# Optimization experiments

Hardware: AMD Instinct MI355X
Metric: run time of the kernel (lower is better)

Reference implementation:

```python
import jax, jax.numpy as jnp
from jax import lax
import numpy as np

D_MODEL, D_STATE, EXPAND, D_CONV = 1024, 16, 2, 4
D_INNER = EXPAND * D_MODEL
B, L = 4, 2048


def setup_inputs() -> dict:
    key = jax.random.key(0)
    ks = jax.random.split(key, 12)
    def xavier(k, shape):
        fan_in, fan_out = shape[1], shape[0]
        lim = float(np.sqrt(6.0 / (fan_in + fan_out)))
        return jax.random.uniform(k, shape, jnp.float32, -lim, lim)
    inp = {}
    inp['x'] = jax.random.normal(ks[0], (B, L, D_MODEL), jnp.float32)
    inp['W_left'] = xavier(ks[1], (D_INNER, D_MODEL))
    inp['conv_w'] = jax.random.normal(ks[2], (D_INNER, 1, D_CONV), jnp.float32) * (1.0 / np.sqrt(D_CONV))
    inp['conv_b'] = jax.random.normal(ks[3], (D_INNER,), jnp.float32) * 0.01
    inp['W_delta'] = jax.random.normal(ks[4], (D_INNER, D_INNER), jnp.float32) * (1.0 / np.sqrt(D_INNER))
    inp['b_delta'] = jnp.zeros((D_INNER,), jnp.float32)
    inp['W_B'] = jax.random.normal(ks[5], (D_STATE, D_INNER), jnp.float32) * (1.0 / np.sqrt(D_INNER))
    inp['W_C'] = jax.random.normal(ks[6], (D_STATE, D_INNER), jnp.float32) * (1.0 / np.sqrt(D_INNER))
    inp['A_log'] = jnp.log(jnp.arange(1, D_STATE + 1, dtype=jnp.float32))
    inp['W_right'] = xavier(ks[7], (D_INNER, D_MODEL))
    inp['ln_g'] = jnp.ones((D_INNER,), jnp.float32)
    inp['ln_b'] = jnp.zeros((D_INNER,), jnp.float32)
    inp['W_out'] = xavier(ks[8], (D_MODEL, D_INNER))
    return inp


def _ssm(xl, W_delta, b_delta, W_B, W_C, A_log):
    # xl: [b, l, d_inner]
    b, l, d_inner = xl.shape
    A = -jax.nn.softplus(A_log)  # [d_state]
    delta = jnp.clip(jax.nn.softplus(xl @ W_delta.T + b_delta), 1e-4, 10.0)
    Bm = xl @ W_B.T  # [b, l, d_state]
    Cm = xl @ W_C.T  # [b, l, d_state]

    def step(h, inp):
        d_t, x_t, B_t, C_t = inp  # [b,d_inner], [b,d_inner], [b,N], [b,N]
        A_bar = jnp.exp(d_t[:, :, None] * A)            # [b, d_inner, N]
        h = A_bar * h + (d_t * x_t)[:, :, None] * B_t[:, None, :]
        y_t = jnp.einsum('bdn,bn->bd', h, C_t)
        return h, y_t

    h0 = jnp.zeros((b, d_inner, A_log.shape[0]), xl.dtype)
    xs = (jnp.swapaxes(delta, 0, 1), jnp.swapaxes(xl, 0, 1),
          jnp.swapaxes(Bm, 0, 1), jnp.swapaxes(Cm, 0, 1))
    _, ys = lax.scan(step, h0, xs)  # ys: [l, b, d_inner]
    return jnp.swapaxes(ys, 0, 1)


def reference(x, W_left, conv_w, conv_b, W_delta, b_delta, W_B, W_C, A_log,
              W_right, ln_g, ln_b, W_out):
    d_conv = conv_w.shape[-1]
    # left branch: linear -> causal depthwise conv1d -> silu
    left = x @ W_left.T                          # [b, l, d_inner]
    left_ncw = jnp.swapaxes(left, 1, 2)          # [b, d_inner, l]
    left_ncw = jnp.pad(left_ncw, ((0, 0), (0, 0), (d_conv - 1, 0)))
    left_ncw = lax.conv_general_dilated(
        left_ncw, conv_w, window_strides=(1,), padding='VALID',
        feature_group_count=conv_w.shape[0]) + conv_b[None, :, None]
    left = jax.nn.silu(jnp.swapaxes(left_ncw, 1, 2))
    # selective scan
    ssm_out = _ssm(left, W_delta, b_delta, W_B, W_C, A_log)
    # right gate (eval mode: dropout off)
    gate = jax.nn.silu(x @ W_right.T)
    out = ssm_out * gate
    # layernorm over d_inner
    mu = jnp.mean(out, axis=-1, keepdims=True)
    var = jnp.mean(jnp.square(out - mu), axis=-1, keepdims=True)
    out = (out - mu) * lax.rsqrt(var + 1e-5) * ln_g + ln_b
    return out @ W_out.T
```

## Files before the change

kernel.cpp:

```cpp
#include <hip/hip_runtime.h>
#include <cstddef>

#define LL 2048
#define TOK 8192
#define DM 1024
#define DI 2048
#define NS 16

typedef _Float16 half_t;
typedef __attribute__((ext_vector_type(8))) _Float16 f16x8;
typedef __attribute__((ext_vector_type(4))) _Float16 f16x4;
typedef __attribute__((ext_vector_type(4))) float f32x4;

__device__ __forceinline__ float softplus_f(float x) {
  return fmaxf(x, 0.f) + log1pf(__expf(-fabsf(x)));
}
__device__ __forceinline__ float silu_f(float x) {
  return x / (1.f + __expf(-x));
}
__device__ __forceinline__ void gload_lds16(const void* g, void* l) {
  __builtin_amdgcn_global_load_lds((const __attribute__((address_space(1))) void*)g,
                                   (__attribute__((address_space(3))) void*)l, 16, 0, 0);
}
#define DPP_ADD(v, ctrl) \
  ((v) + __int_as_float(__builtin_amdgcn_update_dpp(0, __float_as_int(v), (ctrl), 0xf, 0xf, true)))

__device__ float g_buf[120881152];

__global__ __launch_bounds__(256) void f2h_k(const float* __restrict__ in,
                                             half_t* __restrict__ out, int n4) {
  const int i = blockIdx.x * 256 + threadIdx.x;
  if (i >= n4) return;
  const float4 v = ((const float4*)in)[i];
  f16x4 o;
  o[0] = (half_t)v.x; o[1] = (half_t)v.y; o[2] = (half_t)v.z; o[3] = (half_t)v.w;
  ((f16x4*)out)[i] = o;
}

__global__ __launch_bounds__(256) void f2h2_k(const float* __restrict__ in,
                                              half_t* __restrict__ hi,
                                              half_t* __restrict__ lo, int n4) {
  const int i = blockIdx.x * 256 + threadIdx.x;
  if (i >= n4) return;
  const float4 v = ((const float4*)in)[i];
  f16x4 h, l;
  h[0] = (half_t)v.x; h[1] = (half_t)v.y; h[2] = (half_t)v.z; h[3] = (half_t)v.w;
  l[0] = (half_t)(v.x - (float)h[0]);
  l[1] = (half_t)(v.y - (float)h[1]);
  l[2] = (half_t)(v.z - (float)h[2]);
  l[3] = (half_t)(v.w - (float)h[3]);
  ((f16x4*)hi)[i] = h;
  ((f16x4*)lo)[i] = l;
}

template <int ACT>
__global__ __launch_bounds__(256) void gemm_mfma(const half_t* __restrict__ A,
                                                 const half_t* __restrict__ W,
                                                 const float* __restrict__ bias,
                                                 float* __restrict__ C,
                                                 int M, int N, int K) {
  __shared__ half_t lA[4096];
  __shared__ half_t lB[4096];
  const int tid = threadIdx.x;
  const int bm0 = blockIdx.y * 128, bn0 = blockIdx.x * 128;
  const int lane = tid & 63, wave = tid >> 6;
  const int q = lane >> 4, mr = lane & 15;
  const int wm = (wave >> 1) * 64, wn = (wave & 1) * 64;
  const int flat0 = tid, flat1 = tid + 256;
  const int kc0 = flat0 >> 7, r0 = flat0 & 127;
  const int kc1 = flat1 >> 7, r1 = flat1 & 127;

  f32x4 acc[4][4];
#pragma unroll
  for (int i = 0; i < 4; ++i)
#pragma unroll
    for (int j = 0; j < 4; ++j) acc[i][j] = (f32x4){0.f, 0.f, 0.f, 0.f};

  for (int k0 = 0; k0 < K; k0 += 32) {
    gload_lds16(A + (size_t)(bm0 + r0) * K + k0 + kc0 * 8, lA + (size_t)flat0 * 8);
    gload_lds16(A + (size_t)(bm0 + r1) * K + k0 + kc1 * 8, lA + (size_t)flat1 * 8);
    gload_lds16(W + (size_t)(bn0 + r0) * K + k0 + kc0 * 8, lB + (size_t)flat0 * 8);
    gload_lds16(W + (size_t)(bn0 + r1) * K + k0 + kc1 * 8, lB + (size_t)flat1 * 8);
    __syncthreads();
    f16x8 af[4], bg[4];
#pragma unroll
    for (int t = 0; t < 4; ++t) {
      af[t] = *(const f16x8*)(lA + ((q << 10) + ((wm + t * 16 + mr) << 3)));
      bg[t] = *(const f16x8*)(lB + ((q << 10) + ((wn + t * 16 + mr) << 3)));
    }
#pragma unroll
    for (int i = 0; i < 4; ++i)
#pragma unroll
      for (int j = 0; j < 4; ++j)
        acc[i][j] = __builtin_amdgcn_mfma_f32_16x16x32_f16(af[i], bg[j], acc[i][j], 0, 0, 0);
    __syncthreads();
  }

#pragma unroll
  for (int i = 0; i < 4; ++i) {
#pragma unroll
    for (int j = 0; j < 4; ++j) {
      const int col = bn0 + wn + j * 16 + mr;
      const float bv = bias ? bias[col] : 0.f;
#pragma unroll
      for (int r = 0; r < 4; ++r) {
        const int row = bm0 + wm + i * 16 + q * 4 + r;
        float v = acc[i][j][r] + bv;
        if (ACT == 1) v = silu_f(v);
        C[(size_t)row * N + col] = v;
      }
    }
  }
}

__global__ __launch_bounds__(256) void gemm_mfma_lg(const half_t* __restrict__ A,
                                                    const half_t* __restrict__ W,
                                                    float* __restrict__ left,
                                                    float* __restrict__ gate) {
  __shared__ half_t lA[4096];
  __shared__ half_t lB[4096];
  const int tid = threadIdx.x;
  const int bm0 = blockIdx.y * 128, bn0 = blockIdx.x * 128;
  const int K = DM;
  const int lane = tid & 63, wave = tid >> 6;
  const int q = lane >> 4, mr = lane & 15;
  const int wm = (wave >> 1) * 64, wn = (wave & 1) * 64;
  const int flat1 = tid + 256;
  const int kc0 = tid >> 7, r0 = tid & 127;
  const int kc1 = flat1 >> 7, r1 = flat1 & 127;

  f32x4 acc[4][4];
#pragma unroll
  for (int i = 0; i < 4; ++i)
#pragma unroll
    for (int j = 0; j < 4; ++j) acc[i][j] = (f32x4){0.f, 0.f, 0.f, 0.f};

  for (int k0 = 0; k0 < K; k0 += 32) {
    gload_lds16(A + (size_t)(bm0 + r0) * K + k0 + kc0 * 8, lA + (size_t)tid * 8);
    gload_lds16(A + (size_t)(bm0 + r1) * K + k0 + kc1 * 8, lA + (size_t)flat1 * 8);
    gload_lds16(W + (size_t)(bn0 + r0) * K + k0 + kc0 * 8, lB + (size_t)tid * 8);
    gload_lds16(W + (size_t)(bn0 + r1) * K + k0 + kc1 * 8, lB + (size_t)flat1 * 8);
    __syncthreads();
    f16x8 af[4], bg[4];
#pragma unroll
    for (int t = 0; t < 4; ++t) {
      af[t] = *(const f16x8*)(lA + ((q << 10) + ((wm + t * 16 + mr) << 3)));
      bg[t] = *(const f16x8*)(lB + ((q << 10) + ((wn + t * 16 + mr) << 3)));
    }
#pragma unroll
    for (int i = 0; i < 4; ++i)
#pragma unroll
      for (int j = 0; j < 4; ++j)
        acc[i][j] = __builtin_amdgcn_mfma_f32_16x16x32_f16(af[i], bg[j], acc[i][j], 0, 0, 0);
    __syncthreads();
  }

  const int is_gate = (bn0 >= DI);
  float* out = is_gate ? gate : left;
  const int cb = bn0 - (is_gate ? DI : 0);
#pragma unroll
  for (int i = 0; i < 4; ++i) {
#pragma unroll
    for (int j = 0; j < 4; ++j) {
      const int col = cb + wn + j * 16 + mr;
#pragma unroll
      for (int r = 0; r < 4; ++r) {
        const int row = bm0 + wm + i * 16 + q * 4 + r;
        float v = acc[i][j][r];
        if (is_gate) v = silu_f(v);
        out[(size_t)row * DI + col] = v;
      }
    }
  }
}

__global__ __launch_bounds__(512, 4) void gemm_mfma_split(const half_t* __restrict__ Ah,
                                                          const half_t* __restrict__ Wh,
                                                          const half_t* __restrict__ Wl,
                                                          const float* __restrict__ bias,
                                                          float* __restrict__ C,
                                                          int M, int N, int K) {
  __shared__ half_t lAh[8192];
  __shared__ half_t lBh[4096], lBl[4096];
  const int tid = threadIdx.x;
  const int bm0 = blockIdx.y * 256, bn0 = blockIdx.x * 128;
  const int lane = tid & 63, wave = tid >> 6;
  const int q = lane >> 4, mr = lane & 15;
  const int wm = (wave >> 1) * 64, wn = (wave & 1) * 64;
  const int aflat1 = tid + 512;
  const int akc0 = tid >> 8, ar0 = tid & 255;
  const int akc1 = aflat1 >> 8, ar1 = aflat1 & 255;
  const int wkc = tid >> 7, wr = tid & 127;

  f32x4 acc[4][4];
#pragma unroll
  for (int i = 0; i < 4; ++i)
#pragma unroll
    for (int j = 0; j < 4; ++j) acc[i][j] = (f32x4){0.f, 0.f, 0.f, 0.f};

  for (int k0 = 0; k0 < K; k0 += 32) {
    gload_lds16(Ah + (size_t)(bm0 + ar0) * K + k0 + akc0 * 8, lAh + (size_t)tid * 8);
    gload_lds16(Ah + (size_t)(bm0 + ar1) * K + k0 + akc1 * 8, lAh + (size_t)aflat1 * 8);
    gload_lds16(Wh + (size_t)(bn0 + wr) * K + k0 + wkc * 8, lBh + (size_t)tid * 8);
    gload_lds16(Wl + (size_t)(bn0 + wr) * K + k0 + wkc * 8, lBl + (size_t)tid * 8);
    __syncthreads();
    f16x8 ah[4], bh[4], bl[4];
#pragma unroll
    for (int t = 0; t < 4; ++t) {
      const int ao = (q << 11) + ((wm + t * 16 + mr) << 3);
      const int bo = (q << 10) + ((wn + t * 16 + mr) << 3);
      ah[t] = *(const f16x8*)(lAh + ao);
      bh[t] = *(const f16x8*)(lBh + bo);
      bl[t] = *(const f16x8*)(lBl + bo);
    }
#pragma unroll
    for (int i = 0; i < 4; ++i)
#pragma unroll
      for (int j = 0; j < 4; ++j) {
        acc[i][j] = __builtin_amdgcn_mfma_f32_16x16x32_f16(ah[i], bh[j], acc[i][j], 0, 0, 0);
        acc[i][j] = __builtin_amdgcn_mfma_f32_16x16x32_f16(ah[i], bl[j], acc[i][j], 0, 0, 0);
      }
    __syncthreads();
  }

  const int wmg = (wave >> 1) * 64;
#pragma unroll
  for (int i = 0; i < 4; ++i) {
#pragma unroll
    for (int j = 0; j < 4; ++j) {
      const int col = bn0 + wn + j * 16 + mr;
      const float bv = bias[col];
#pragma unroll
      for (int r = 0; r < 4; ++r) {
        const int row = bm0 + wmg + i * 16 + q * 4 + r;
        float v = softplus_f(acc[i][j][r] + bv);
        v = fminf(fmaxf(v, 1e-4f), 10.f);
        C[(size_t)row * N + col] = v;
      }
    }
  }
}

__global__ __launch_bounds__(256) void bc_mfma(const half_t* __restrict__ A,
                                               const half_t* __restrict__ Wbc,
                                               float* __restrict__ bc) {
  __shared__ half_t lA[4096];
  __shared__ half_t lB[1024];
  const int tid = threadIdx.x;
  const int bm0 = blockIdx.x * 128;
  const int lane = tid & 63, wave = tid >> 6;
  const int q = lane >> 4, mr = lane & 15;
  const int wm = wave * 32;
  const int flat1 = tid + 256;
  const int kcA0 = tid >> 7, rA0 = tid & 127;
  const int kcA1 = flat1 >> 7, rA1 = flat1 & 127;
  const int kcB = tid >> 5, rB = tid & 31;

  f32x4 acc[2][2];
#pragma unroll
  for (int i = 0; i < 2; ++i)
#pragma unroll
    for (int j = 0; j < 2; ++j) acc[i][j] = (f32x4){0.f, 0.f, 0.f, 0.f};

  for (int k0 = 0; k0 < DI; k0 += 32) {
    gload_lds16(A + (size_t)(bm0 + rA0) * DI + k0 + kcA0 * 8, lA + (size_t)tid * 8);
    gload_lds16(A + (size_t)(bm0 + rA1) * DI + k0 + kcA1 * 8, lA + (size_t)flat1 * 8);
    if (tid < 128)
      gload_lds16(Wbc + (size_t)rB * DI + k0 + kcB * 8, lB + (size_t)tid * 8);
    __syncthreads();
    f16x8 af[2], bg[2];
#pragma unroll
    for (int t = 0; t < 2; ++t) {
      af[t] = *(const f16x8*)(lA + ((q << 10) + ((wm + t * 16 + mr) << 3)));
      bg[t] = *(const f16x8*)(lB + ((q << 8) + ((t * 16 + mr) << 3)));
    }
#pragma unroll
    for (int i = 0; i < 2; ++i)
#pragma unroll
      for (int j = 0; j < 2; ++j)
        acc[i][j] = __builtin_amdgcn_mfma_f32_16x16x32_f16(af[i], bg[j], acc[i][j], 0, 0, 0);
    __syncthreads();
  }

#pragma unroll
  for (int i = 0; i < 2; ++i) {
#pragma unroll
    for (int j = 0; j < 2; ++j) {
#pragma unroll
      for (int r = 0; r < 4; ++r) {
        const int row = bm0 + wm + i * 16 + q * 4 + r;
        bc[(size_t)row * 32 + 2 * mr + j] = acc[i][j][r];
      }
    }
  }
}

__global__ __launch_bounds__(256) void conv_silu_k(const float* __restrict__ left,
                                                   const float* __restrict__ cw,
                                                   const float* __restrict__ cb,
                                                   float* __restrict__ xc,
                                                   half_t* __restrict__ xch) {
  const int idx = blockIdx.x * 256 + threadIdx.x;
  const int d = idx & (DI - 1);
  const int bt = idx >> 11;
  const int t = bt & (LL - 1);
  const float4 wv = *(const float4*)(cw + (size_t)d * 4);
  float acc = cb[d];
  const size_t base = (size_t)idx;
  if (t >= 3) {
    acc += left[base - 3 * DI] * wv.x + left[base - 2 * DI] * wv.y +
           left[base - DI] * wv.z + left[base] * wv.w;
  } else {
    acc += left[base] * wv.w;
    if (t >= 1) acc += left[base - DI] * wv.z;
    if (t >= 2) acc += left[base - 2 * DI] * wv.y;
  }
  const float v = silu_f(acc);
  xc[base] = v;
  xch[base] = (half_t)v;
}

#define ST 32
__global__ __launch_bounds__(256) void scan_k(const float* __restrict__ delta,
                                              const float* __restrict__ xc,
                                              const float* __restrict__ gate,
                                              const float* __restrict__ bcp,
                                              const float* __restrict__ A_log,
                                              float* __restrict__ y) {
  __shared__ float dx2[16 * 68];
  __shared__ float bcs[ST * 32];
  __shared__ float ys[ST * 16];
  const int tid = threadIdx.x;
  const int b  = blockIdx.x >> 7;
  const int d0 = (blockIdx.x & 127) << 4;
  const int n  = tid & 15;
  const int ch = tid >> 4;
  const float An = -softplus_f(A_log[n]);

  const int t_a = tid >> 4, c_a = tid & 15;
  const int t_b = t_a + 16;

  float h = 0.f;
  const size_t batch_base = (size_t)b * LL * DI + d0;
  const size_t batch_bc   = (size_t)b * LL * 32;

  size_t rb_cur = batch_base;
  float g0, g1;
  {
    const size_t ra = rb_cur + (size_t)t_a * DI + c_a;
    const size_t rbx = rb_cur + (size_t)t_b * DI + c_a;
    const float d0v = delta[ra], x0v = xc[ra];
    const float d1v = delta[rbx], x1v = xc[rbx];
    g0 = gate[ra]; g1 = gate[rbx];
    const float2 b0 = *(const float2*)&bcp[batch_bc + (size_t)t_a * 32 + 2 * c_a];
    const float2 b1 = *(const float2*)&bcp[batch_bc + (size_t)t_b * 32 + 2 * c_a];
    *(float2*)&dx2[c_a * 68 + t_a * 2] = make_float2(d0v, x0v);
    *(float2*)&dx2[c_a * 68 + t_b * 2] = make_float2(d1v, x1v);
    *(float2*)&bcs[t_a * 32 + 2 * c_a] = b0;
    *(float2*)&bcs[t_b * 32 + 2 * c_a] = b1;
  }
  __syncthreads();

  for (int it = 0; it < LL / ST; ++it) {
    float nd0, nx0, ng0, nd1, nx1, ng1;
    float2 nb0, nb1;
    const size_t rb_nxt = batch_base + (size_t)(it + 1) * ST * DI;
    if (it + 1 < LL / ST) {
      const size_t ra = rb_nxt + (size_t)t_a * DI + c_a;
      const size_t rbx = rb_nxt + (size_t)t_b * DI + c_a;
      nd0 = delta[ra]; nx0 = xc[ra]; ng0 = gate[ra];
      nd1 = delta[rbx]; nx1 = xc[rbx]; ng1 = gate[rbx];
      const size_t bcb = batch_bc + (size_t)(it + 1) * ST * 32;
      nb0 = *(const float2*)&bcp[bcb + (size_t)t_a * 32 + 2 * c_a];
      nb1 = *(const float2*)&bcp[bcb + (size_t)t_b * 32 + 2 * c_a];
    }

    const float* dxp = &dx2[ch * 68];
#pragma unroll
    for (int tt = 0; tt < ST; tt += 2) {
      const float4 v = *(const float4*)&dxp[tt * 2];
      const float2 bc0 = *(const float2*)&bcs[tt * 32 + 2 * n];
      const float2 bc1 = *(const float2*)&bcs[(tt + 1) * 32 + 2 * n];
      float ab = __expf(v.x * An);
      h = fmaf(ab, h, v.x * v.y * bc0.x);
      float p = h * bc0.y;
      p = DPP_ADD(p, 0x111); p = DPP_ADD(p, 0x112);
      p = DPP_ADD(p, 0x114); p = DPP_ADD(p, 0x118);
      if (n == 15) ys[tt * 16 + ch] = p;
      ab = __expf(v.z * An);
      h = fmaf(ab, h, v.z * v.w * bc1.x);
      p = h * bc1.y;
      p = DPP_ADD(p, 0x111); p = DPP_ADD(p, 0x112);
      p = DPP_ADD(p, 0x114); p = DPP_ADD(p, 0x118);
      if (n == 15) ys[(tt + 1) * 16 + ch] = p;
    }
    __syncthreads();

    if (it + 1 < LL / ST) {
      *(float2*)&dx2[c_a * 68 + t_a * 2] = make_float2(nd0, nx0);
      *(float2*)&dx2[c_a * 68 + t_b * 2] = make_float2(nd1, nx1);
      *(float2*)&bcs[t_a * 32 + 2 * c_a] = nb0;
      *(float2*)&bcs[t_b * 32 + 2 * c_a] = nb1;
    }
    y[rb_cur + (size_t)t_a * DI + c_a] = ys[t_a * 16 + c_a] * g0;
    y[rb_cur + (size_t)t_b * DI + c_a] = ys[t_b * 16 + c_a] * g1;
    g0 = ng0; g1 = ng1;
    rb_cur = rb_nxt;
    __syncthreads();
  }
}

__global__ __launch_bounds__(256) void ln_k(const float* __restrict__ y,
                                            const float* __restrict__ gam,
                                            const float* __restrict__ bet,
                                            half_t* __restrict__ outn) {
  const int row = blockIdx.x;
  const int tid = threadIdx.x;
  const float* yr = y + (size_t)row * DI;
  const float4 v0 = ((const float4*)yr)[tid];
  const float4 v1 = ((const float4*)yr)[tid + 256];
  float s = v0.x + v0.y + v0.z + v0.w + v1.x + v1.y + v1.z + v1.w;
  float q = v0.x * v0.x + v0.y * v0.y + v0.z * v0.z + v0.w * v0.w +
            v1.x * v1.x + v1.y * v1.y + v1.z * v1.z + v1.w * v1.w;
  for (int off = 32; off > 0; off >>= 1) {
    s += __shfl_down(s, off);
    q += __shfl_down(q, off);
  }
  __shared__ float sred[4], qred[4];
  const int wid = tid >> 6;
  if ((tid & 63) == 0) { sred[wid] = s; qred[wid] = q; }
  __syncthreads();
  s = sred[0] + sred[1] + sred[2] + sred[3];
  q = qred[0] + qred[1] + qred[2] + qred[3];
  const float mu = s * (1.f / DI);
  const float rs = rsqrtf(q * (1.f / DI) - mu * mu + 1e-5f);
  half_t* orow = outn + (size_t)row * DI;
  const int c0 = tid * 4, c1 = (tid + 256) * 4;
  f16x4 o;
  o[0] = (half_t)((v0.x - mu) * rs * gam[c0 + 0] + bet[c0 + 0]);
  o[1] = (half_t)((v0.y - mu) * rs * gam[c0 + 1] + bet[c0 + 1]);
  o[2] = (half_t)((v0.z - mu) * rs * gam[c0 + 2] + bet[c0 + 2]);
  o[3] = (half_t)((v0.w - mu) * rs * gam[c0 + 3] + bet[c0 + 3]);
  ((f16x4*)orow)[tid] = o;
  o[0] = (half_t)((v1.x - mu) * rs * gam[c1 + 0] + bet[c1 + 0]);
  o[1] = (half_t)((v1.y - mu) * rs * gam[c1 + 1] + bet[c1 + 1]);
  o[2] = (half_t)((v1.z - mu) * rs * gam[c1 + 2] + bet[c1 + 2]);
  o[3] = (half_t)((v1.w - mu) * rs * gam[c1 + 3] + bet[c1 + 3]);
  ((f16x4*)orow)[tid + 256] = o;
}

extern "C" void kernel_launch(void* const* d_in, const int* in_sizes, int n_in,
                              void* d_out, int out_size, void* d_ws, size_t ws_size,
                              hipStream_t stream) {
  const float* x       = (const float*)d_in[0];
  const float* W_left  = (const float*)d_in[1];
  const float* conv_w  = (const float*)d_in[2];
  const float* conv_b  = (const float*)d_in[3];
  const float* W_delta = (const float*)d_in[4];
  const float* b_delta = (const float*)d_in[5];
  const float* W_B     = (const float*)d_in[6];
  const float* W_C     = (const float*)d_in[7];
  const float* A_log   = (const float*)d_in[8];
  const float* W_right = (const float*)d_in[9];
  const float* ln_g    = (const float*)d_in[10];
  const float* ln_b    = (const float*)d_in[11];
  const float* W_out   = (const float*)d_in[12];

  float* buf = nullptr;
  hipGetSymbolAddress((void**)&buf, HIP_SYMBOL(g_buf));
  half_t* xh   = (half_t*)(buf + 0);
  half_t* wlgh = (half_t*)(buf + 4194304);
  half_t* wrh  = (half_t*)(buf + 5242880);
  half_t* wdh  = (half_t*)(buf + 6291456);
  half_t* wdl  = (half_t*)(buf + 8388608);
  half_t* woh  = (half_t*)(buf + 10485760);
  float* left  = buf + 11534336;
  float* xc    = buf + 28311552;
  half_t* xch  = (half_t*)(buf + 45088768);
  float* dlt   = buf + 61865984;
  float* gate  = buf + 78643200;
  float* yv    = buf + 95420416;
  half_t* nrmh = (half_t*)(buf + 112197632);
  float* bc    = buf + 120586240;
  half_t* wbch = (half_t*)(buf + 120848384);

  f2h_k<<<8192, 256, 0, stream>>>(x, xh, TOK * DM / 4);
  f2h_k<<<2048, 256, 0, stream>>>(W_left, wlgh, DI * DM / 4);
  f2h_k<<<2048, 256, 0, stream>>>(W_right, wrh, DI * DM / 4);
  f2h_k<<<2048, 256, 0, stream>>>(W_out, woh, DM * DI / 4);
  f2h2_k<<<4096, 256, 0, stream>>>(W_delta, wdh, wdl, DI * DI / 4);
  f2h_k<<<32, 256, 0, stream>>>(W_B, wbch, NS * DI / 4);
  f2h_k<<<32, 256, 0, stream>>>(W_C, wbch + NS * DI, NS * DI / 4);

  gemm_mfma_lg<<<dim3(2 * DI / 128, TOK / 128), 256, 0, stream>>>(xh, wlgh, left, gate);
  conv_silu_k<<<TOK * DI / 256, 256, 0, stream>>>(left, conv_w, conv_b, xc, xch);
  gemm_mfma_split<<<dim3(DI / 128, TOK / 256), 512, 0, stream>>>(xch, wdh, wdl, b_delta, dlt, TOK, DI, DI);
  bc_mfma<<<TOK / 128, 256, 0, stream>>>(xch, wbch, bc);
  scan_k<<<512, 256, 0, stream>>>(dlt, xc, gate, bc, A_log, yv);
  ln_k<<<TOK, 256, 0, stream>>>(yv, ln_g, ln_b, nrmh);
  gemm_mfma<0><<<dim3(DM / 128, TOK / 128), 256, 0, stream>>>(nrmh, woh, nullptr, (float*)d_out, TOK, DM, DI);
}
```

Measured before the change: 930.4 us.

## Double-buffer and enlarge delta split-GEMM tile to 256x256 with MFMA priority

```diff
diff --git a/kernel.cpp b/kernel.cpp
--- a/kernel.cpp
+++ b/kernel.cpp
@@ -174,65 +174,87 @@
   }
 }
 
-__global__ __launch_bounds__(512, 4) void gemm_mfma_split(const half_t* __restrict__ Ah,
+__global__ __launch_bounds__(512, 2) void gemm_mfma_split(const half_t* __restrict__ Ah,
                                                           const half_t* __restrict__ Wh,
                                                           const half_t* __restrict__ Wl,
                                                           const float* __restrict__ bias,
                                                           float* __restrict__ C,
                                                           int M, int N, int K) {
-  __shared__ half_t lAh[8192];
-  __shared__ half_t lBh[4096], lBl[4096];
+  __shared__ half_t lAh[2][8192];
+  __shared__ half_t lBh[2][8192];
+  __shared__ half_t lBl[2][8192];
   const int tid = threadIdx.x;
-  const int bm0 = blockIdx.y * 256, bn0 = blockIdx.x * 128;
+  const int bm0 = blockIdx.y * 256, bn0 = blockIdx.x * 256;
   const int lane = tid & 63, wave = tid >> 6;
   const int q = lane >> 4, mr = lane & 15;
-  const int wm = (wave >> 1) * 64, wn = (wave & 1) * 64;
-  const int aflat1 = tid + 512;
-  const int akc0 = tid >> 8, ar0 = tid & 255;
-  const int akc1 = aflat1 >> 8, ar1 = aflat1 & 255;
-  const int wkc = tid >> 7, wr = tid & 127;
-
-  f32x4 acc[4][4];
-#pragma unroll
-  for (int i = 0; i < 4; ++i)
+  const int wm = (wave >> 2) * 128, wn = (wave & 3) * 64;
+  const int f0 = tid, f1 = tid + 512;
+  const int kc0 = f0 >> 8, r0 = f0 & 255;
+  const int kc1 = f1 >> 8, r1 = f1 & 255;
+
+#define STAGE_S(bufp, kk)                                                            \
+  do {                                                                               \
+    gload_lds16(Ah + (size_t)(bm0 + r0) * K + (kk) + kc0 * 8, lAh[bufp] + f0 * 8);   \
+    gload_lds16(Ah + (size_t)(bm0 + r1) * K + (kk) + kc1 * 8, lAh[bufp] + f1 * 8);   \
+    gload_lds16(Wh + (size_t)(bn0 + r0) * K + (kk) + kc0 * 8, lBh[bufp] + f0 * 8);   \
+    gload_lds16(Wh + (size_t)(bn0 + r1) * K + (kk) + kc1 * 8, lBh[bufp] + f1 * 8);   \
+    gload_lds16(Wl + (size_t)(bn0 + r0) * K + (kk) + kc0 * 8, lBl[bufp] + f0 * 8);   \
+    gload_lds16(Wl + (size_t)(bn0 + r1) * K + (kk) + kc1 * 8, lBl[bufp] + f1 * 8);   \
+  } while (0)
+
+  f32x4 acc[8][4];
+#pragma unroll
+  for (int i = 0; i < 8; ++i)
 #pragma unroll
     for (int j = 0; j < 4; ++j) acc[i][j] = (f32x4){0.f, 0.f, 0.f, 0.f};
 
+  STAGE_S(0, 0);
+  __syncthreads();
+
+  int cur = 0;
   for (int k0 = 0; k0 < K; k0 += 32) {
-    gload_lds16(Ah + (size_t)(bm0 + ar0) * K + k0 + akc0 * 8, lAh + (size_t)tid * 8);
-    gload_lds16(Ah + (size_t)(bm0 + ar1) * K + k0 + akc1 * 8, lAh + (size_t)aflat1 * 8);
-    gload_lds16(Wh + (size_t)(bn0 + wr) * K + k0 + wkc * 8, lBh + (size_t)tid * 8);
-    gload_lds16(Wl + (size_t)(bn0 + wr) * K + k0 + wkc * 8, lBl + (size_t)tid * 8);
-    __syncthreads();
-    f16x8 ah[4], bh[4], bl[4];
-#pragma unroll
-    for (int t = 0; t < 4; ++t) {
-      const int ao = (q << 11) + ((wm + t * 16 + mr) << 3);
-      const int bo = (q << 10) + ((wn + t * 16 + mr) << 3);
-      ah[t] = *(const f16x8*)(lAh + ao);
-      bh[t] = *(const f16x8*)(lBh + bo);
-      bl[t] = *(const f16x8*)(lBl + bo);
-    }
-#pragma unroll
-    for (int i = 0; i < 4; ++i)
-#pragma unroll
-      for (int j = 0; j < 4; ++j) {
-        acc[i][j] = __builtin_amdgcn_mfma_f32_16x16x32_f16(ah[i], bh[j], acc[i][j], 0, 0, 0);
-        acc[i][j] = __builtin_amdgcn_mfma_f32_16x16x32_f16(ah[i], bl[j], acc[i][j], 0, 0, 0);
-      }
-    __syncthreads();
-  }
-
-  const int wmg = (wave >> 1) * 64;
-#pragma unroll
-  for (int i = 0; i < 4; ++i) {
+    if (k0 + 32 < K) STAGE_S(cur ^ 1, k0 + 32);
+
+    const int qb = q << 11;
+    const f16x8* pA = (const f16x8*)(lAh[cur] + qb);
+    const f16x8* pBh = (const f16x8*)(lBh[cur] + qb);
+    const f16x8* pBl = (const f16x8*)(lBl[cur] + qb);
+    f16x8 ah[8], bh4[4], bl4[4];
+#pragma unroll
+    for (int j = 0; j < 4; ++j) {
+      bh4[j] = pBh[wn + j * 16 + mr];
+      bl4[j] = pBl[wn + j * 16 + mr];
+    }
+#pragma unroll
+    for (int i = 0; i < 8; ++i) ah[i] = pA[wm + i * 16 + mr];
+
+    __builtin_amdgcn_s_setprio(1);
+#pragma unroll
+    for (int i = 0; i < 8; ++i)
+#pragma unroll
+      for (int j = 0; j < 4; ++j)
+        acc[i][j] = __builtin_amdgcn_mfma_f32_16x16x32_f16(ah[i], bh4[j], acc[i][j], 0, 0, 0);
+#pragma unroll
+    for (int i = 0; i < 8; ++i)
+#pragma unroll
+      for (int j = 0; j < 4; ++j)
+        acc[i][j] = __builtin_amdgcn_mfma_f32_16x16x32_f16(ah[i], bl4[j], acc[i][j], 0, 0, 0);
+    __builtin_amdgcn_s_setprio(0);
+
+    __syncthreads();
+    cur ^= 1;
+  }
+#undef STAGE_S
+
+#pragma unroll
+  for (int i = 0; i < 8; ++i) {
 #pragma unroll
     for (int j = 0; j < 4; ++j) {
       const int col = bn0 + wn + j * 16 + mr;
       const float bv = bias[col];
 #pragma unroll
       for (int r = 0; r < 4; ++r) {
-        const int row = bm0 + wmg + i * 16 + q * 4 + r;
+        const int row = bm0 + wm + i * 16 + q * 4 + r;
         float v = softplus_f(acc[i][j][r] + bv);
         v = fminf(fmaxf(v, 1e-4f), 10.f);
         C[(size_t)row * N + col] = v;
@@ -494,7 +516,7 @@
 
   gemm_mfma_lg<<<dim3(2 * DI / 128, TOK / 128), 256, 0, stream>>>(xh, wlgh, left, gate);
   conv_silu_k<<<TOK * DI / 256, 256, 0, stream>>>(left, conv_w, conv_b, xc, xch);
-  gemm_mfma_split<<<dim3(DI / 128, TOK / 256), 512, 0, stream>>>(xch, wdh, wdl, b_delta, dlt, TOK, DI, DI);
+  gemm_mfma_split<<<dim3(DI / 256, TOK / 256), 512, 0, stream>>>(xch, wdh, wdl, b_delta, dlt, TOK, DI, DI);
   bc_mfma<<<TOK / 128, 256, 0, stream>>>(xch, wbch, bc);
   scan_k<<<512, 256, 0, stream>>>(dlt, xc, gate, bc, A_log, yv);
   ln_k<<<TOK, 256, 0, stream>>>(yv, ln_g, ln_b, nrmh);
```

Result: slower. 1.637 ms (+75.9%).

## Retile delta GEMM to 128x128 blocks with swizzled block order and MFMA priority

Applied to the files above, without the earlier changes.

```diff
diff --git a/kernel.cpp b/kernel.cpp
--- a/kernel.cpp
+++ b/kernel.cpp
@@ -174,23 +174,26 @@
   }
 }
 
-__global__ __launch_bounds__(512, 4) void gemm_mfma_split(const half_t* __restrict__ Ah,
+__global__ __launch_bounds__(256, 4) void gemm_mfma_split(const half_t* __restrict__ Ah,
                                                           const half_t* __restrict__ Wh,
                                                           const half_t* __restrict__ Wl,
                                                           const float* __restrict__ bias,
                                                           float* __restrict__ C,
                                                           int M, int N, int K) {
-  __shared__ half_t lAh[8192];
-  __shared__ half_t lBh[4096], lBl[4096];
+  __shared__ half_t lA[4096];
+  __shared__ half_t lBh[4096];
+  __shared__ half_t lBl[4096];
   const int tid = threadIdx.x;
-  const int bm0 = blockIdx.y * 256, bn0 = blockIdx.x * 128;
+  const int flat = blockIdx.y * gridDim.x + blockIdx.x;
+  const int lo = (flat >> 3) | ((flat & 7) << 7);
+  const int bn0 = (lo & 15) << 7;
+  const int bm0 = (lo >> 4) << 7;
   const int lane = tid & 63, wave = tid >> 6;
   const int q = lane >> 4, mr = lane & 15;
   const int wm = (wave >> 1) * 64, wn = (wave & 1) * 64;
-  const int aflat1 = tid + 512;
-  const int akc0 = tid >> 8, ar0 = tid & 255;
-  const int akc1 = aflat1 >> 8, ar1 = aflat1 & 255;
-  const int wkc = tid >> 7, wr = tid & 127;
+  const int flat1 = tid + 256;
+  const int kc0 = tid >> 7, r0 = tid & 127;
+  const int kc1 = flat1 >> 7, r1 = flat1 & 127;
 
   f32x4 acc[4][4];
 #pragma unroll
@@ -199,31 +202,34 @@
     for (int j = 0; j < 4; ++j) acc[i][j] = (f32x4){0.f, 0.f, 0.f, 0.f};
 
   for (int k0 = 0; k0 < K; k0 += 32) {
-    gload_lds16(Ah + (size_t)(bm0 + ar0) * K + k0 + akc0 * 8, lAh + (size_t)tid * 8);
-    gload_lds16(Ah + (size_t)(bm0 + ar1) * K + k0 + akc1 * 8, lAh + (size_t)aflat1 * 8);
-    gload_lds16(Wh + (size_t)(bn0 + wr) * K + k0 + wkc * 8, lBh + (size_t)tid * 8);
-    gload_lds16(Wl + (size_t)(bn0 + wr) * K + k0 + wkc * 8, lBl + (size_t)tid * 8);
-    __syncthreads();
-    f16x8 ah[4], bh[4], bl[4];
+    gload_lds16(Ah + (size_t)(bm0 + r0) * K + k0 + kc0 * 8, lA + (size_t)tid * 8);
+    gload_lds16(Ah + (size_t)(bm0 + r1) * K + k0 + kc1 * 8, lA + (size_t)flat1 * 8);
+    gload_lds16(Wh + (size_t)(bn0 + r0) * K + k0 + kc0 * 8, lBh + (size_t)tid * 8);
+    gload_lds16(Wh + (size_t)(bn0 + r1) * K + k0 + kc1 * 8, lBh + (size_t)flat1 * 8);
+    gload_lds16(Wl + (size_t)(bn0 + r0) * K + k0 + kc0 * 8, lBl + (size_t)tid * 8);
+    gload_lds16(Wl + (size_t)(bn0 + r1) * K + k0 + kc1 * 8, lBl + (size_t)flat1 * 8);
+    __syncthreads();
+    f16x8 af[4], bh[4], bl[4];
 #pragma unroll
     for (int t = 0; t < 4; ++t) {
-      const int ao = (q << 11) + ((wm + t * 16 + mr) << 3);
-      const int bo = (q << 10) + ((wn + t * 16 + mr) << 3);
-      ah[t] = *(const f16x8*)(lAh + ao);
-      bh[t] = *(const f16x8*)(lBh + bo);
-      bl[t] = *(const f16x8*)(lBl + bo);
-    }
+      const int o = (q << 10) + ((wm + t * 16 + mr) << 3);
+      const int ob = (q << 10) + ((wn + t * 16 + mr) << 3);
+      af[t] = *(const f16x8*)(lA + o);
+      bh[t] = *(const f16x8*)(lBh + ob);
+      bl[t] = *(const f16x8*)(lBl + ob);
+    }
+    __builtin_amdgcn_s_setprio(1);
 #pragma unroll
     for (int i = 0; i < 4; ++i)
 #pragma unroll
       for (int j = 0; j < 4; ++j) {
-        acc[i][j] = __builtin_amdgcn_mfma_f32_16x16x32_f16(ah[i], bh[j], acc[i][j], 0, 0, 0);
-        acc[i][j] = __builtin_amdgcn_mfma_f32_16x16x32_f16(ah[i], bl[j], acc[i][j], 0, 0, 0);
+        acc[i][j] = __builtin_amdgcn_mfma_f32_16x16x32_f16(af[i], bh[j], acc[i][j], 0, 0, 0);
+        acc[i][j] = __builtin_amdgcn_mfma_f32_16x16x32_f16(af[i], bl[j], acc[i][j], 0, 0, 0);
       }
-    __syncthreads();
-  }
-
-  const int wmg = (wave >> 1) * 64;
+    __builtin_amdgcn_s_setprio(0);
+    __syncthreads();
+  }
+
 #pragma unroll
   for (int i = 0; i < 4; ++i) {
 #pragma unroll
@@ -232,7 +238,7 @@
       const float bv = bias[col];
 #pragma unroll
       for (int r = 0; r < 4; ++r) {
-        const int row = bm0 + wmg + i * 16 + q * 4 + r;
+        const int row = bm0 + wm + i * 16 + q * 4 + r;
         float v = softplus_f(acc[i][j][r] + bv);
         v = fminf(fmaxf(v, 1e-4f), 10.f);
         C[(size_t)row * N + col] = v;
@@ -494,7 +500,7 @@
 
   gemm_mfma_lg<<<dim3(2 * DI / 128, TOK / 128), 256, 0, stream>>>(xh, wlgh, left, gate);
   conv_silu_k<<<TOK * DI / 256, 256, 0, stream>>>(left, conv_w, conv_b, xc, xch);
-  gemm_mfma_split<<<dim3(DI / 128, TOK / 256), 512, 0, stream>>>(xch, wdh, wdl, b_delta, dlt, TOK, DI, DI);
+  gemm_mfma_split<<<dim3(DI / 128, TOK / 128), 256, 0, stream>>>(xch, wdh, wdl, b_delta, dlt, TOK, DI, DI);
   bc_mfma<<<TOK / 128, 256, 0, stream>>>(xch, wbch, bc);
   scan_k<<<512, 256, 0, stream>>>(dlt, xc, gate, bc, A_log, yv);
   ln_k<<<TOK, 256, 0, stream>>>(yv, ln_g, ln_b, nrmh);
```

New measurement: 1.013 ms. +8.9%, slower.

## Drop hi/lo split for delta GEMM and fuse B/C projection into it

Applied to the files above, without the earlier changes.

```diff
diff --git a/kernel.cpp b/kernel.cpp
--- a/kernel.cpp
+++ b/kernel.cpp
@@ -37,20 +37,12 @@
   ((f16x4*)out)[i] = o;
 }
 
-__global__ __launch_bounds__(256) void f2h2_k(const float* __restrict__ in,
-                                              half_t* __restrict__ hi,
-                                              half_t* __restrict__ lo, int n4) {
+__global__ __launch_bounds__(256) void zh_k(half_t* __restrict__ out, int n4) {
   const int i = blockIdx.x * 256 + threadIdx.x;
   if (i >= n4) return;
-  const float4 v = ((const float4*)in)[i];
-  f16x4 h, l;
-  h[0] = (half_t)v.x; h[1] = (half_t)v.y; h[2] = (half_t)v.z; h[3] = (half_t)v.w;
-  l[0] = (half_t)(v.x - (float)h[0]);
-  l[1] = (half_t)(v.y - (float)h[1]);
-  l[2] = (half_t)(v.z - (float)h[2]);
-  l[3] = (half_t)(v.w - (float)h[3]);
-  ((f16x4*)hi)[i] = h;
-  ((f16x4*)lo)[i] = l;
+  f16x4 o;
+  o[0] = (half_t)0.f; o[1] = (half_t)0.f; o[2] = (half_t)0.f; o[3] = (half_t)0.f;
+  ((f16x4*)out)[i] = o;
 }
 
 template <int ACT>
@@ -174,16 +166,16 @@
   }
 }
 
-__global__ __launch_bounds__(512, 4) void gemm_mfma_split(const half_t* __restrict__ Ah,
-                                                          const half_t* __restrict__ Wh,
-                                                          const half_t* __restrict__ Wl,
-                                                          const float* __restrict__ bias,
-                                                          float* __restrict__ C,
-                                                          int M, int N, int K) {
-  __shared__ half_t lAh[8192];
-  __shared__ half_t lBh[4096], lBl[4096];
+__global__ __launch_bounds__(512, 4) void gemm_delta_bc(const half_t* __restrict__ A,
+                                                        const half_t* __restrict__ W,
+                                                        const float* __restrict__ bias,
+                                                        float* __restrict__ dlt,
+                                                        float* __restrict__ bcout) {
+  __shared__ half_t lA[8192];
+  __shared__ half_t lB[4096];
   const int tid = threadIdx.x;
   const int bm0 = blockIdx.y * 256, bn0 = blockIdx.x * 128;
+  const int K = DI;
   const int lane = tid & 63, wave = tid >> 6;
   const int q = lane >> 4, mr = lane & 15;
   const int wm = (wave >> 1) * 64, wn = (wave & 1) * 64;
@@ -199,97 +191,58 @@
     for (int j = 0; j < 4; ++j) acc[i][j] = (f32x4){0.f, 0.f, 0.f, 0.f};
 
   for (int k0 = 0; k0 < K; k0 += 32) {
-    gload_lds16(Ah + (size_t)(bm0 + ar0) * K + k0 + akc0 * 8, lAh + (size_t)tid * 8);
-    gload_lds16(Ah + (size_t)(bm0 + ar1) * K + k0 + akc1 * 8, lAh + (size_t)aflat1 * 8);
-    gload_lds16(Wh + (size_t)(bn0 + wr) * K + k0 + wkc * 8, lBh + (size_t)tid * 8);
-    gload_lds16(Wl + (size_t)(bn0 + wr) * K + k0 + wkc * 8, lBl + (size_t)tid * 8);
-    __syncthreads();
-    f16x8 ah[4], bh[4], bl[4];
+    gload_lds16(A + (size_t)(bm0 + ar0) * K + k0 + akc0 * 8, lA + (size_t)tid * 8);
+    gload_lds16(A + (size_t)(bm0 + ar1) * K + k0 + akc1 * 8, lA + (size_t)aflat1 * 8);
+    gload_lds16(W + (size_t)(bn0 + wr) * K + k0 + wkc * 8, lB + (size_t)tid * 8);
+    __syncthreads();
+    f16x8 ah[4], bg[4];
 #pragma unroll
     for (int t = 0; t < 4; ++t) {
       const int ao = (q << 11) + ((wm + t * 16 + mr) << 3);
       const int bo = (q << 10) + ((wn + t * 16 + mr) << 3);
-      ah[t] = *(const f16x8*)(lAh + ao);
-      bh[t] = *(const f16x8*)(lBh + bo);
-      bl[t] = *(const f16x8*)(lBl + bo);
-    }
+      ah[t] = *(const f16x8*)(lA + ao);
+      bg[t] = *(const f16x8*)(lB + bo);
+    }
+    __builtin_amdgcn_s_setprio(1);
 #pragma unroll
     for (int i = 0; i < 4; ++i)
 #pragma unroll
+      for (int j = 0; j < 4; ++j)
+        acc[i][j] = __builtin_amdgcn_mfma_f32_16x16x32_f16(ah[i], bg[j], acc[i][j], 0, 0, 0);
+    __builtin_amdgcn_s_setprio(0);
+    __syncthreads();
+  }
+
+  if (bn0 < DI) {
+#pragma unroll
+    for (int i = 0; i < 4; ++i) {
+#pragma unroll
       for (int j = 0; j < 4; ++j) {
-        acc[i][j] = __builtin_amdgcn_mfma_f32_16x16x32_f16(ah[i], bh[j], acc[i][j], 0, 0, 0);
-        acc[i][j] = __builtin_amdgcn_mfma_f32_16x16x32_f16(ah[i], bl[j], acc[i][j], 0, 0, 0);
+        const int col = bn0 + wn + j * 16 + mr;
+        const float bv = bias[col];
+#pragma unroll
+        for (int r = 0; r < 4; ++r) {
+          const int row = bm0 + wm + i * 16 + q * 4 + r;
+          float v = softplus_f(acc[i][j][r] + bv);
+          v = fminf(fmaxf(v, 1e-4f), 10.f);
+          dlt[(size_t)row * DI + col] = v;
+        }
       }
-    __syncthreads();
-  }
-
-  const int wmg = (wave >> 1) * 64;
-#pragma unroll
-  for (int i = 0; i < 4; ++i) {
-#pragma unroll
-    for (int j = 0; j < 4; ++j) {
-      const int col = bn0 + wn + j * 16 + mr;
-      const float bv = bias[col];
-#pragma unroll
-      for (int r = 0; r < 4; ++r) {
-        const int row = bm0 + wmg + i * 16 + q * 4 + r;
-        float v = softplus_f(acc[i][j][r] + bv);
-        v = fminf(fmaxf(v, 1e-4f), 10.f);
-        C[(size_t)row * N + col] = v;
-      }
-    }
-  }
-}
-
-__global__ __launch_bounds__(256) void bc_mfma(const half_t* __restrict__ A,
-                                               const half_t* __restrict__ Wbc,
-                                               float* __restrict__ bc) {
-  __shared__ half_t lA[4096];
-  __shared__ half_t lB[1024];
-  const int tid = threadIdx.x;
-  const int bm0 = blockIdx.x * 128;
-  const int lane = tid & 63, wave = tid >> 6;
-  const int q = lane >> 4, mr = lane & 15;
-  const int wm = wave * 32;
-  const int flat1 = tid + 256;
-  const int kcA0 = tid >> 7, rA0 = tid & 127;
-  const int kcA1 = flat1 >> 7, rA1 = flat1 & 127;
-  const int kcB = tid >> 5, rB = tid & 31;
-
-  f32x4 acc[2][2];
-#pragma unroll
-  for (int i = 0; i < 2; ++i)
-#pragma unroll
-    for (int j = 0; j < 2; ++j) acc[i][j] = (f32x4){0.f, 0.f, 0.f, 0.f};
-
-  for (int k0 = 0; k0 < DI; k0 += 32) {
-    gload_lds16(A + (size_t)(bm0 + rA0) * DI + k0 + kcA0 * 8, lA + (size_t)tid * 8);
-    gload_lds16(A + (size_t)(bm0 + rA1) * DI + k0 + kcA1 * 8, lA + (size_t)flat1 * 8);
-    if (tid < 128)
-      gload_lds16(Wbc + (size_t)rB * DI + k0 + kcB * 8, lB + (size_t)tid * 8);
-    __syncthreads();
-    f16x8 af[2], bg[2];
-#pragma unroll
-    for (int t = 0; t < 2; ++t) {
-      af[t] = *(const f16x8*)(lA + ((q << 10) + ((wm + t * 16 + mr) << 3)));
-      bg[t] = *(const f16x8*)(lB + ((q << 8) + ((t * 16 + mr) << 3)));
-    }
-#pragma unroll
-    for (int i = 0; i < 2; ++i)
-#pragma unroll
-      for (int j = 0; j < 2; ++j)
-        acc[i][j] = __builtin_amdgcn_mfma_f32_16x16x32_f16(af[i], bg[j], acc[i][j], 0, 0, 0);
-    __syncthreads();
-  }
-
-#pragma unroll
-  for (int i = 0; i < 2; ++i) {
-#pragma unroll
-    for (int j = 0; j < 2; ++j) {
-#pragma unroll
-      for (int r = 0; r < 4; ++r) {
-        const int row = bm0 + wm + i * 16 + q * 4 + r;
-        bc[(size_t)row * 32 + 2 * mr + j] = acc[i][j][r];
+    }
+  } else {
+#pragma unroll
+    for (int i = 0; i < 4; ++i) {
+#pragma unroll
+      for (int j = 0; j < 4; ++j) {
+        const int c = wn + j * 16 + mr;
+        if (c < 32) {
+          const int slot = (c < 16) ? (2 * c) : (2 * (c - 16) + 1);
+#pragma unroll
+          for (int r = 0; r < 4; ++r) {
+            const int row = bm0 + wm + i * 16 + q * 4 + r;
+            bcout[(size_t)row * 32 + slot] = acc[i][j][r];
+          }
+        }
       }
     }
   }
@@ -471,8 +424,7 @@
   half_t* xh   = (half_t*)(buf + 0);
   half_t* wlgh = (half_t*)(buf + 4194304);
   half_t* wrh  = (half_t*)(buf + 5242880);
-  half_t* wdh  = (half_t*)(buf + 6291456);
-  half_t* wdl  = (half_t*)(buf + 8388608);
+  half_t* wdf  = (half_t*)(buf + 6291456);
   half_t* woh  = (half_t*)(buf + 10485760);
   float* left  = buf + 11534336;
   float* xc    = buf + 28311552;
@@ -482,20 +434,19 @@
   float* yv    = buf + 95420416;
   half_t* nrmh = (half_t*)(buf + 112197632);
   float* bc    = buf + 120586240;
-  half_t* wbch = (half_t*)(buf + 120848384);
 
   f2h_k<<<8192, 256, 0, stream>>>(x, xh, TOK * DM / 4);
   f2h_k<<<2048, 256, 0, stream>>>(W_left, wlgh, DI * DM / 4);
   f2h_k<<<2048, 256, 0, stream>>>(W_right, wrh, DI * DM / 4);
   f2h_k<<<2048, 256, 0, stream>>>(W_out, woh, DM * DI / 4);
-  f2h2_k<<<4096, 256, 0, stream>>>(W_delta, wdh, wdl, DI * DI / 4);
-  f2h_k<<<32, 256, 0, stream>>>(W_B, wbch, NS * DI / 4);
-  f2h_k<<<32, 256, 0, stream>>>(W_C, wbch + NS * DI, NS * DI / 4);
+  f2h_k<<<4096, 256, 0, stream>>>(W_delta, wdf, DI * DI / 4);
+  f2h_k<<<32, 256, 0, stream>>>(W_B, wdf + (size_t)DI * DI, NS * DI / 4);
+  f2h_k<<<32, 256, 0, stream>>>(W_C, wdf + (size_t)(DI + NS) * DI, NS * DI / 4);
+  zh_k<<<192, 256, 0, stream>>>(wdf + (size_t)(DI + 2 * NS) * DI, 96 * DI / 4);
 
   gemm_mfma_lg<<<dim3(2 * DI / 128, TOK / 128), 256, 0, stream>>>(xh, wlgh, left, gate);
   conv_silu_k<<<TOK * DI / 256, 256, 0, stream>>>(left, conv_w, conv_b, xc, xch);
-  gemm_mfma_split<<<dim3(DI / 128, TOK / 256), 512, 0, stream>>>(xch, wdh, wdl, b_delta, dlt, TOK, DI, DI);
-  bc_mfma<<<TOK / 128, 256, 0, stream>>>(xch, wbch, bc);
+  gemm_delta_bc<<<dim3(17, TOK / 256), 512, 0, stream>>>(xch, wdf, b_delta, dlt, bc);
   scan_k<<<512, 256, 0, stream>>>(dlt, xc, gate, bc, A_log, yv);
   ln_k<<<TOK, 256, 0, stream>>>(yv, ln_g, ln_b, nrmh);
   gemm_mfma<0><<<dim3(DM / 128, TOK / 128), 256, 0, stream>>>(nrmh, woh, nullptr, (float*)d_out, TOK, DM, DI);
```

Result: faster. 909.2 us, median of 2 (-2.3%).
